# Kernel optimization log

Measured on AMD Instinct MI355X. Metric: run time of the kernel, lower is better.

The kernel has to match this reference:

```python
import jax, jax.numpy as jnp
import numpy as np

IFZ = 256      # in_features
SFZ = 1280     # sequence_features
AHZ = 8        # attention heads
AFZ = 64       # attention feature dim per head
NRES = 20      # canonical_num_residues
SCALE = float(np.sqrt(AFZ))
RESID = float(np.sqrt(2.0))
EPS = 1e-6


def _ln(x, s, b, eps=1e-5):
    m = jnp.mean(x, axis=-1, keepdims=True)
    v = jnp.var(x, axis=-1, keepdims=True)
    return (x - m) / jnp.sqrt(v + eps) * s + b


def setup_inputs() -> dict:
    key = jax.random.key(0)
    ks = jax.random.split(key, 20)
    N, B, S = 4096, 4, 512
    HD = AHZ * AFZ
    w = lambda k, shp: (jax.random.normal(k, shp, jnp.float32) * 0.02)
    d = {}
    d["x"] = jax.random.normal(ks[0], (N, IFZ), jnp.float32)
    d["packed_sequence_emb"] = jax.random.normal(ks[1], (B, S, SFZ), jnp.float32)
    d["packed_sequence_mask"] = jnp.ones((B, S), jnp.float32)
    d["prot_mask"] = jnp.arange(N, dtype=jnp.int32)
    d["batch"] = jax.random.randint(ks[2], (N,), 0, B, jnp.int32)
    # projections (bias=False)
    d["Wq"] = w(ks[3], (HD, IFZ))
    d["Wk"] = w(ks[4], (HD, SFZ))
    d["Wv"] = w(ks[5], (HD, SFZ))
    # ag: LayerNorm(HD) -> Linear(HD, IFZ, bias=False) (dropout = identity at eval)
    d["ag_ln_s"] = jnp.ones((HD,), jnp.float32)
    d["ag_ln_b"] = jnp.zeros((HD,), jnp.float32)
    d["Wag"] = w(ks[6], (IFZ, HD))
    d["res_ln_s"] = jnp.ones((3, IFZ), jnp.float32)
    d["res_ln_b"] = jnp.zeros((3, IFZ), jnp.float32)
    d["res_w1"] = w(ks[7], (3, IFZ, IFZ))
    d["res_b1"] = jnp.zeros((3, IFZ), jnp.float32)
    d["res_w2"] = w(ks[8], (3, IFZ, IFZ))
    d["res_b2"] = jnp.zeros((3, IFZ), jnp.float32)
    d["head_w"] = w(ks[9], (NRES, IFZ))
    d["head_b"] = jnp.zeros((NRES,), jnp.float32)
    # output LayerNorm en
    d["en_s"] = jnp.ones((IFZ,), jnp.float32)
    d["en_b"] = jnp.zeros((IFZ,), jnp.float32)
    return d


def _forward(x, emb, mask, prot_mask, batch, Wq, Wk, Wv, ag_ln_s, ag_ln_b, Wag,
             res_ln_s, res_ln_b, res_w1, res_b1, res_w2, res_b2,
             head_w, head_b, en_s, en_b):
    N = x.shape[0]
    B, S = emb.shape[:2]
    b_idx = batch[prot_mask]                      # [M]
    xp = x[prot_mask]                             # [M, IFZ]
    M = xp.shape[0]
    q = (xp @ Wq.T).reshape(M, AHZ, AFZ)          # [M,H,D]
    k = (emb @ Wk.T).reshape(B, S, AHZ, AFZ)      # [B,S,H,D]
    v = (emb @ Wv.T).reshape(B, S, AHZ, AFZ)
    # score vs every protein, then pick own protein (avoids materializing [M,S,H,D] gather)
    scores_all = jnp.einsum('mhd,bshd->mbsh', q, k) / SCALE          # [M,B,S,H]
    sel = b_idx[:, None, None, None]
    scores = jnp.take_along_axis(scores_all, sel, axis=1)[:, 0]       # [M,S,H]
    mb = mask[b_idx][:, :, None]                                      # [M,S,1]
    # padded_sequence_softmax: softmax over S, zero pads, renormalize
    sm = jax.nn.softmax(scores, axis=1) * mb
    w = sm / (jnp.sum(sm, axis=1, keepdims=True) + EPS)               # [M,S,H]
    feat_all = jnp.einsum('msh,bshd->mbhd', w, v)                     # [M,B,H,D]
    feat = jnp.take_along_axis(feat_all, sel, axis=1)[:, 0]
    feat = feat.reshape(M, AHZ * AFZ)
    ag = _ln(feat, ag_ln_s, ag_ln_b) @ Wag.T                          # [M, IFZ]
    # seq_aa_head on the scattered new features (identical to ag for unique prot_mask)
    h = ag
    for i in range(3):
        y = _ln(h, res_ln_s[i], res_ln_b[i])
        y = jax.nn.relu(y @ res_w1[i].T + res_b1[i])
        y = y @ res_w2[i].T + res_b2[i]
        h = (h + y) / RESID
    logits = h @ head_w.T + head_b                                     # [M, NRES]
    new_features = jnp.zeros_like(x).at[prot_mask].set(ag)
    seq_aa_logits = jnp.zeros((N, NRES), x.dtype).at[prot_mask].set(logits)
    unpacked_scores = jnp.zeros((N, S, AHZ), x.dtype).at[prot_mask].set(scores)
    out_x = _ln(x + new_features / RESID, en_s, en_b)
    return out_x, seq_aa_logits, unpacked_scores


def reference(x, packed_sequence_emb, packed_sequence_mask, prot_mask, batch,
              Wq, Wk, Wv, ag_ln_s, ag_ln_b, Wag,
              res_ln_s, res_ln_b, res_w1, res_b1, res_w2, res_b2,
              head_w, head_b, en_s, en_b):
    return _forward(x, packed_sequence_emb, packed_sequence_mask, prot_mask, batch,
                    Wq, Wk, Wv, ag_ln_s, ag_ln_b, Wag,
                    res_ln_s, res_ln_b, res_w1, res_b1, res_w2, res_b2,
                    head_w, head_b, en_s, en_b)
```

## Files before the change

### kernel.cpp

```cpp
#include <hip/hip_runtime.h>
#include <math.h>


typedef short bf8 __attribute__((ext_vector_type(8)));
typedef short bf4 __attribute__((ext_vector_type(4)));
typedef float f32x4 __attribute__((ext_vector_type(4)));
typedef unsigned short u16;

constexpr int LDT = 40;
enum { EPI_NONE = 0, EPI_BIAS_RELU = 1, EPI_BIAS = 2, EPI_RESID = 3 };
#define RSQRT2 0.70710678118654752f

__device__ __forceinline__ u16 f2bf(float f) {
  unsigned int u = __builtin_bit_cast(unsigned int, f);
  unsigned int r = u + 0x7fffu + ((u >> 16) & 1u);
  return (u16)(r >> 16);
}
__device__ __forceinline__ float bf2f(u16 v) {
  return __builtin_bit_cast(float, (unsigned int)v << 16);
}
__device__ __forceinline__ f32x4 mfma16(bf8 a, bf8 b, f32x4 c) {
  return __builtin_amdgcn_mfma_f32_16x16x32_bf16(a, b, c, 0, 0, 0);
}

struct CvtDesc { const float* src; u16* dst; int n; };
struct CvtArgs { CvtDesc d[8]; };

__global__ __launch_bounds__(256) void cvt_k(CvtArgs a) {
  CvtDesc d = a.d[blockIdx.z];
  int i = (blockIdx.x * 256 + threadIdx.x) * 8;
  if (i >= d.n) return;
  f32x4 v0 = *(const f32x4*)(d.src + i);
  f32x4 v1 = *(const f32x4*)(d.src + i + 4);
  bf8 o;
  o[0] = (short)f2bf(v0[0]); o[1] = (short)f2bf(v0[1]);
  o[2] = (short)f2bf(v0[2]); o[3] = (short)f2bf(v0[3]);
  o[4] = (short)f2bf(v1[0]); o[5] = (short)f2bf(v1[1]);
  o[6] = (short)f2bf(v1[2]); o[7] = (short)f2bf(v1[3]);
  *(bf8*)(d.dst + i) = o;
}

template <int EPI, bool BFOUT, int MT>
__global__ __launch_bounds__(256) void mgemm2(
    const u16* __restrict__ A, const u16* __restrict__ B,
    void* __restrict__ Cv, int M, int N, int K, int lda, int ldb, int ldc,
    const float* __restrict__ bias, const float* __restrict__ Hin,
    const int* __restrict__ gatherA, const int* __restrict__ scatterC) {
  constexpr int NF = MT / 32;
  __shared__ __align__(16) u16 As[MT * LDT];
  __shared__ __align__(16) u16 Bs[64 * LDT];
  const int tid = threadIdx.x;
  const int m0 = blockIdx.y * MT, n0 = blockIdx.x * 64;
  const int wave = tid >> 6, lane = tid & 63;
  const int wm = (wave & 1) * (MT / 2), wn = (wave >> 1) * 32;
  const int lrow = lane & 15, quad = lane >> 4;
  const int srow = tid >> 2, skq = tid & 3;

  int gr0 = m0 + srow;
  int ar0 = (gr0 < M) ? (gatherA ? gatherA[gr0] : gr0) : -1;
  const u16* Ap0 = (ar0 >= 0) ? A + (size_t)ar0 * lda + skq * 8 : nullptr;
  const u16* Ap1 = nullptr;
  if constexpr (MT == 128) {
    int gr1 = m0 + srow + 64;
    int ar1 = (gr1 < M) ? (gatherA ? gatherA[gr1] : gr1) : -1;
    Ap1 = (ar1 >= 0) ? A + (size_t)ar1 * lda + skq * 8 : nullptr;
  }
  const u16* Bp = (n0 + srow < N) ? B + (size_t)(n0 + srow) * ldb + skq * 8 : nullptr;
  u16* AsW0 = &As[srow * LDT + skq * 8];
  u16* AsW1 = (MT == 128) ? &As[(srow + 64) * LDT + skq * 8] : nullptr;
  u16* BsW = &Bs[srow * LDT + skq * 8];

  f32x4 acc[NF][2];
#pragma unroll
  for (int i = 0; i < NF; ++i)
#pragma unroll
    for (int j = 0; j < 2; ++j) acc[i][j] = (f32x4){0.f, 0.f, 0.f, 0.f};
  const bf8 z8 = {0, 0, 0, 0, 0, 0, 0, 0};

  for (int k0 = 0; k0 < K; k0 += 32) {
    bf8 a0 = Ap0 ? *(const bf8*)(Ap0 + k0) : z8;
    bf8 bv = Bp ? *(const bf8*)(Bp + k0) : z8;
    *(bf8*)AsW0 = a0;
    if constexpr (MT == 128) {
      bf8 a1 = Ap1 ? *(const bf8*)(Ap1 + k0) : z8;
      *(bf8*)AsW1 = a1;
    }
    *(bf8*)BsW = bv;
    __syncthreads();
    bf8 af[NF], bfr[2];
#pragma unroll
    for (int i = 0; i < NF; ++i)
      af[i] = *(const bf8*)&As[(wm + i * 16 + lrow) * LDT + quad * 8];
#pragma unroll
    for (int j = 0; j < 2; ++j)
      bfr[j] = *(const bf8*)&Bs[(wn + j * 16 + lrow) * LDT + quad * 8];
#pragma unroll
    for (int i = 0; i < NF; ++i)
#pragma unroll
      for (int j = 0; j < 2; ++j) acc[i][j] = mfma16(af[i], bfr[j], acc[i][j]);
    __syncthreads();
  }

  float* Cf = (float*)Cv;
  u16* Cb = (u16*)Cv;
#pragma unroll
  for (int i = 0; i < NF; ++i) {
#pragma unroll
    for (int r = 0; r < 4; ++r) {
      int row = m0 + wm + i * 16 + quad * 4 + r;
      if (row >= M) continue;
      if (gatherA && gatherA[row] < 0) continue;
      int orow = scatterC ? scatterC[row] : row;
#pragma unroll
      for (int j = 0; j < 2; ++j) {
        int col = n0 + wn + j * 16 + lrow;
        if (col >= N) continue;
        float v = acc[i][j][r];
        if (EPI == EPI_BIAS_RELU) v = fmaxf(v + bias[col], 0.f);
        else if (EPI == EPI_BIAS) v += bias[col];
        else if (EPI == EPI_RESID) v = (Hin[(size_t)row * ldc + col] + v + bias[col]) * RSQRT2;
        if (BFOUT) Cb[(size_t)orow * ldc + col] = f2bf(v);
        else Cf[(size_t)orow * ldc + col] = v;
      }
    }
  }
}

__global__ __launch_bounds__(256) void vtrans(const u16* __restrict__ KV,
                                              u16* __restrict__ VT) {
  __shared__ u16 t[32][33];
  int b = blockIdx.z;
  int s0 = blockIdx.x * 32, d0 = blockIdx.y * 32;
  int tx = threadIdx.x & 31, ty = threadIdx.x >> 5;
#pragma unroll
  for (int i = 0; i < 32; i += 8)
    t[ty + i][tx] = KV[(size_t)(b * 512 + s0 + ty + i) * 1024 + 512 + d0 + tx];
  __syncthreads();
#pragma unroll
  for (int i = 0; i < 32; i += 8)
    VT[(size_t)(b * 512 + d0 + ty + i) * 512 + s0 + tx] = t[tx][ty + i];
}

constexpr int WST = 520;
constexpr int QST = 72;

__global__ __launch_bounds__(256) void attn_fused(
    const u16* __restrict__ Q, const u16* __restrict__ KV,
    const u16* __restrict__ VT, const int* __restrict__ list,
    const float* __restrict__ mask, u16* __restrict__ packed,
    u16* __restrict__ feat, int N) {
  const int NMT = gridDim.x;
  const int lin = blockIdx.y * NMT + blockIdx.x;
  const int xcd = lin & 7, rest = lin >> 3;
  const int mt = rest % NMT;
  const int y = ((rest / NMT) << 3) | xcd;
  const int b = y >> 3, h = y & 7;
  const int* lst = list + (size_t)b * N + mt * 32;
  if (lst[0] < 0) return;

  __shared__ __align__(16) u16 Ws[32 * WST];
  __shared__ __align__(16) u16 KVs[2][64 * QST];
  __shared__ int mS[32];

  const int tid = threadIdx.x;
  const int wave = tid >> 6, lane = tid & 63;
  const int wm = (wave & 1) * 16, wns = (wave >> 1) * 32;
  const int lrow = lane & 15, quad = lane >> 4;
  const bf8 z8 = {0, 0, 0, 0, 0, 0, 0, 0};

  const int c0 = tid * 2, c1 = tid * 2 + 1;
  const int sr0 = c0 >> 3, kq0 = c0 & 7;
  const int sr1 = c1 >> 3, kq1 = c1 & 7;
  const int o0 = sr0 * QST + kq0 * 8, o1 = sr1 * QST + kq1 * 8;

  const u16* KVb = KV + (size_t)(b * 512) * 1024 + h * 64;
  const u16* VTb = VT + (size_t)(b * 512 + h * 64) * 512;

  if (tid < 32) mS[tid] = lst[tid];
  {
    int sta = mt & 7;
    *(bf8*)&KVs[0][o0] = *(const bf8*)(KVb + (size_t)(sta * 64 + sr0) * 1024 + kq0 * 8);
    *(bf8*)&KVs[0][o1] = *(const bf8*)(KVb + (size_t)(sta * 64 + sr1) * 1024 + kq1 * 8);
  }
  __syncthreads();

  const int qrow = mS[wm + lrow];
  const u16* Qr = Q + (size_t)qrow * 512 + h * 64 + quad * 8;
  const bf8 qa0 = (qrow >= 0) ? *(const bf8*)Qr : z8;
  const bf8 qa1 = (qrow >= 0) ? *(const bf8*)(Qr + 32) : z8;

  int cur = 0;
  bf8 r0, r1;
  for (int st = 0; st < 8; ++st) {
    const int sta = (st + mt) & 7;
    if (st < 7) {
      int nx = (st + 1 + mt) & 7;
      r0 = *(const bf8*)(KVb + (size_t)(nx * 64 + sr0) * 1024 + kq0 * 8);
      r1 = *(const bf8*)(KVb + (size_t)(nx * 64 + sr1) * 1024 + kq1 * 8);
    }
    f32x4 acc0 = {0.f, 0.f, 0.f, 0.f}, acc1 = acc0;
    {
      bf8 b00 = *(const bf8*)&KVs[cur][(wns + lrow) * QST + quad * 8];
      bf8 b10 = *(const bf8*)&KVs[cur][(wns + 16 + lrow) * QST + quad * 8];
      bf8 b01 = *(const bf8*)&KVs[cur][(wns + lrow) * QST + 32 + quad * 8];
      bf8 b11 = *(const bf8*)&KVs[cur][(wns + 16 + lrow) * QST + 32 + quad * 8];
      __builtin_amdgcn_s_setprio(1);
      acc0 = mfma16(qa0, b00, acc0);
      acc1 = mfma16(qa0, b10, acc1);
      acc0 = mfma16(qa1, b01, acc0);
      acc1 = mfma16(qa1, b11, acc1);
      __builtin_amdgcn_s_setprio(0);
    }
#pragma unroll
    for (int r = 0; r < 4; ++r) {
      int lr = wm + quad * 4 + r;
      Ws[lr * WST + sta * 64 + wns + lrow] = f2bf(acc0[r] * 0.125f);
      Ws[lr * WST + sta * 64 + wns + 16 + lrow] = f2bf(acc1[r] * 0.125f);
    }
    if (st < 7) {
      *(bf8*)&KVs[cur ^ 1][o0] = r0;
      *(bf8*)&KVs[cur ^ 1][o1] = r1;
    }
    __syncthreads();
    cur ^= 1;
  }

  bf8 v0p = *(const bf8*)(VTb + (size_t)sr0 * 512 + ((mt & 7) << 6) + kq0 * 8);
  bf8 v1p = *(const bf8*)(VTb + (size_t)sr1 * 512 + ((mt & 7) << 6) + kq1 * 8);

  {
    const int row = tid >> 3, part = tid & 7;
    u16* wrow = &Ws[row * WST + part * 64];
    const int mm = mS[row];
    const float* mkp = mask + (size_t)b * 512 + part * 64;
    bf8 w[8];
    float mx = -1e30f;
#pragma unroll
    for (int v = 0; v < 8; ++v) {
      w[v] = *(const bf8*)(wrow + v * 8);
#pragma unroll
      for (int j = 0; j < 8; ++j) mx = fmaxf(mx, bf2f((u16)w[v][j]));
    }
    if (mm >= 0) {
      u16* prow = packed + ((size_t)h * N + mm) * 512 + part * 64;
#pragma unroll
      for (int v = 0; v < 8; ++v) *(bf8*)(prow + v * 8) = w[v];
    }
#pragma unroll
    for (int d = 1; d < 8; d <<= 1) mx = fmaxf(mx, __shfl_xor(mx, d));
    float ev[64];
    float se = 0.f, ms = 0.f;
#pragma unroll
    for (int v = 0; v < 8; ++v) {
      f32x4 m0 = *(const f32x4*)(mkp + v * 8);
      f32x4 m1 = *(const f32x4*)(mkp + v * 8 + 4);
#pragma unroll
      for (int j = 0; j < 8; ++j) {
        float e = __expf(bf2f((u16)w[v][j]) - mx);
        ev[v * 8 + j] = e;
        se += e;
        ms += e * (j < 4 ? m0[j] : m1[j - 4]);
      }
    }
#pragma unroll
    for (int d = 1; d < 8; d <<= 1) {
      se += __shfl_xor(se, d);
      ms += __shfl_xor(ms, d);
    }
    float iv = 1.0f / (ms + 1e-6f * se);
#pragma unroll
    for (int v = 0; v < 8; ++v) {
      f32x4 m0 = *(const f32x4*)(mkp + v * 8);
      f32x4 m1 = *(const f32x4*)(mkp + v * 8 + 4);
      bf8 o;
#pragma unroll
      for (int j = 0; j < 8; ++j)
        o[j] = (short)f2bf(ev[v * 8 + j] * (j < 4 ? m0[j] : m1[j - 4]) * iv);
      *(bf8*)(wrow + v * 8) = o;
    }
  }
  __syncthreads();
  *(bf8*)&KVs[0][o0] = v0p;
  *(bf8*)&KVs[0][o1] = v1p;
  __syncthreads();

  f32x4 acc0 = {0.f, 0.f, 0.f, 0.f}, acc1 = acc0;
  cur = 0;
  for (int ss = 0; ss < 8; ++ss) {
    const int s0 = ((ss + mt) & 7) << 6;
    if (ss < 7) {
      int nx = ((ss + 1 + mt) & 7) << 6;
      v0p = *(const bf8*)(VTb + (size_t)sr0 * 512 + nx + kq0 * 8);
      v1p = *(const bf8*)(VTb + (size_t)sr1 * 512 + nx + kq1 * 8);
    }
#pragma unroll
    for (int k0 = 0; k0 < 64; k0 += 32) {
      bf8 a = *(const bf8*)&Ws[(wm + lrow) * WST + s0 + k0 + quad * 8];
      bf8 b0 = *(const bf8*)&KVs[cur][(wns + lrow) * QST + k0 + quad * 8];
      bf8 b1 = *(const bf8*)&KVs[cur][(wns + 16 + lrow) * QST + k0 + quad * 8];
      __builtin_amdgcn_s_setprio(1);
      acc0 = mfma16(a, b0, acc0);
      acc1 = mfma16(a, b1, acc1);
      __builtin_amdgcn_s_setprio(0);
    }
    if (ss < 7) {
      *(bf8*)&KVs[cur ^ 1][o0] = v0p;
      *(bf8*)&KVs[cur ^ 1][o1] = v1p;
      __syncthreads();
    }
    cur ^= 1;
  }
#pragma unroll
  for (int r = 0; r < 4; ++r) {
    int lr = wm + quad * 4 + r;
    int mm = mS[lr];
    if (mm < 0) continue;
    u16* frow = feat + (size_t)mm * 512 + h * 64;
    frow[wns + lrow] = f2bf(acc0[r]);
    frow[wns + 16 + lrow] = f2bf(acc1[r]);
  }
}

__global__ __launch_bounds__(256) void unpack_k(const u16* __restrict__ packed,
                                                const int* __restrict__ pm,
                                                float* __restrict__ out_sc,
                                                int N) {
  __shared__ u16 Ls[8 * 520];
  int m = blockIdx.x, tid = threadIdx.x;
  int h = tid >> 5, c = (tid & 31) * 16;
  const u16* row = packed + ((size_t)h * N + m) * 512 + c;
  *(bf8*)&Ls[h * 520 + c] = *(const bf8*)row;
  *(bf8*)&Ls[h * 520 + c + 8] = *(const bf8*)(row + 8);
  __syncthreads();
  float* orow = out_sc + (size_t)pm[m] * 4096;
#pragma unroll
  for (int i = 0; i < 16; ++i) {
    int e = tid + i * 256;
    orow[e] = bf2f(Ls[(e & 7) * 520 + (e >> 3)]);
  }
}

constexpr int HST = 268;
constexpr int AST = 520;
constexpr int YST = 280;

__global__ __launch_bounds__(1024) void mlp_fused(
    const u16* __restrict__ feat, const float* __restrict__ ag_s,
    const float* __restrict__ ag_b, const u16* __restrict__ Wag,
    const float* __restrict__ x, const float* __restrict__ ens,
    const float* __restrict__ enb, const float* __restrict__ rls,
    const float* __restrict__ rlb, const u16* __restrict__ rw1,
    const float* __restrict__ rb1, const u16* __restrict__ rw2,
    const float* __restrict__ rb2, const float* __restrict__ hw,
    const float* __restrict__ hb, const int* __restrict__ pm,
    float* __restrict__ out_lg, float* __restrict__ out_x) {
  __shared__ __align__(16) float Hs[16 * HST];
  __shared__ __align__(16) u16 As[16 * AST];
  __shared__ __align__(16) u16 Ys[16 * YST];
  const int tid = threadIdx.x;
  const int m0 = blockIdx.x * 16;
  const int wave = tid >> 6, lane = tid & 63;
  const int lrow = lane & 15, quad = lane >> 4;
  const int wn = wave * 16;
  const int row = wave;
  const int wq8 = quad * 8;
  const int nrow = pm[m0 + row];

  const u16* WagW = Wag + (size_t)(wn + lrow) * 512 + wq8;
  const u16* W1W = rw1 + (size_t)(wn + lrow) * 256 + wq8;
  const u16* W2W = rw2 + (size_t)(wn + lrow) * 256 + wq8;

  bf8 wp[8];
#pragma unroll
  for (int i = 0; i < 8; ++i) wp[i] = *(const bf8*)(WagW + i * 32);

  {
    const u16* frow = feat + (size_t)(m0 + row) * 512 + lane * 8;
    bf8 f0 = *(const bf8*)frow;
    float s = 0.f, sq = 0.f;
#pragma unroll
    for (int j = 0; j < 8; ++j) {
      float a = bf2f((u16)f0[j]);
      s += a;
      sq += a * a;
    }
#pragma unroll
    for (int d = 1; d < 64; d <<= 1) { s += __shfl_xor(s, d); sq += __shfl_xor(sq, d); }
    float mean = s * (1.0f / 512.0f);
    float var = sq * (1.0f / 512.0f) - mean * mean;
    float is = 1.0f / sqrtf(var + 1e-5f);
    int c = lane * 8;
    bf8 o0;
#pragma unroll
    for (int j = 0; j < 8; ++j)
      o0[j] = (short)f2bf((bf2f((u16)f0[j]) - mean) * is * ag_s[c + j] + ag_b[c + j]);
    *(bf8*)&As[row * AST + c] = o0;
  }
  __syncthreads();

  {
    f32x4 acc = {0.f, 0.f, 0.f, 0.f};
#pragma unroll
    for (int i = 0; i < 8; ++i) {
      bf8 a = *(const bf8*)&As[lrow * AST + i * 32 + wq8];
      acc = mfma16(a, wp[i], acc);
      wp[i] = *(const bf8*)(WagW + 256 + i * 32);
    }
#pragma unroll
    for (int i = 0; i < 8; ++i) {
      bf8 a = *(const bf8*)&As[lrow * AST + 256 + i * 32 + wq8];
      acc = mfma16(a, wp[i], acc);
      wp[i] = *(const bf8*)(W1W + i * 32);
    }
#pragma unroll
    for (int r = 0; r < 4; ++r) {
      int rr = quad * 4 + r;
      Hs[rr * HST + wn + lrow] = acc[r];
    }
  }
  __syncthreads();

  {
    int c = lane * 4;
    f32x4 xv = *(const f32x4*)&x[(size_t)nrow * 256 + c];
    f32x4 hv = *(const f32x4*)&Hs[row * HST + c];
    f32x4 v;
#pragma unroll
    for (int e = 0; e < 4; ++e) v[e] = xv[e] + hv[e] * RSQRT2;
    float s = v[0] + v[1] + v[2] + v[3];
    float sq = v[0] * v[0] + v[1] * v[1] + v[2] * v[2] + v[3] * v[3];
#pragma unroll
    for (int d = 1; d < 64; d <<= 1) { s += __shfl_xor(s, d); sq += __shfl_xor(sq, d); }
    float mean = s * (1.0f / 256.0f);
    float var = sq * (1.0f / 256.0f) - mean * mean;
    float is = 1.0f / sqrtf(var + 1e-5f);
    f32x4 o;
#pragma unroll
    for (int e = 0; e < 4; ++e)
      o[e] = (v[e] - mean) * is * ens[c + e] + enb[c + e];
    *(f32x4*)&out_x[(size_t)nrow * 256 + c] = o;
  }

  for (int layer = 0; layer < 3; ++layer) {
    {
      int c = lane * 4;
      f32x4 h0 = *(const f32x4*)&Hs[row * HST + c];
      float s = h0[0] + h0[1] + h0[2] + h0[3];
      float sq = h0[0] * h0[0] + h0[1] * h0[1] + h0[2] * h0[2] + h0[3] * h0[3];
#pragma unroll
      for (int d = 1; d < 64; d <<= 1) { s += __shfl_xor(s, d); sq += __shfl_xor(sq, d); }
      float mean = s * (1.0f / 256.0f);
      float var = sq * (1.0f / 256.0f) - mean * mean;
      float is = 1.0f / sqrtf(var + 1e-5f);
      const float* g = rls + layer * 256;
      const float* bb = rlb + layer * 256;
      bf4 o;
#pragma unroll
      for (int e = 0; e < 4; ++e)
        o[e] = (short)f2bf((h0[e] - mean) * is * g[c + e] + bb[c + e]);
      *(bf4*)&As[row * AST + c] = o;
    }
    __syncthreads();

    {
      f32x4 acc = {0.f, 0.f, 0.f, 0.f};
#pragma unroll
      for (int i = 0; i < 8; ++i) {
        bf8 a = *(const bf8*)&As[lrow * AST + i * 32 + wq8];
        acc = mfma16(a, wp[i], acc);
        wp[i] = *(const bf8*)(W2W + (size_t)layer * 65536 + i * 32);
      }
      float bi = rb1[layer * 256 + wn + lrow];
#pragma unroll
      for (int r = 0; r < 4; ++r) {
        int rr = quad * 4 + r;
        Ys[rr * YST + wn + lrow] = f2bf(fmaxf(acc[r] + bi, 0.f));
      }
    }
    __syncthreads();

    {
      f32x4 acc = {0.f, 0.f, 0.f, 0.f};
#pragma unroll
      for (int i = 0; i < 8; ++i) {
        bf8 a = *(const bf8*)&Ys[lrow * YST + i * 32 + wq8];
        acc = mfma16(a, wp[i], acc);
        if (layer < 2)
          wp[i] = *(const bf8*)(W1W + (size_t)(layer + 1) * 65536 + i * 32);
      }
      float bi = rb2[layer * 256 + wn + lrow];
#pragma unroll
      for (int r = 0; r < 4; ++r) {
        int rr = quad * 4 + r;
        float* h0 = &Hs[rr * HST + wn + lrow];
        *h0 = (*h0 + acc[r] + bi) * RSQRT2;
      }
    }
    __syncthreads();
  }

  if (lane < 20) {
    const float* hrow = &Hs[row * HST];
    const float* wrow = hw + (size_t)lane * 256;
    float l0 = 0.f, l1 = 0.f, l2 = 0.f, l3 = 0.f;
    for (int k = 0; k < 256; k += 16) {
      f32x4 h0 = *(const f32x4*)&hrow[k];
      f32x4 h1 = *(const f32x4*)&hrow[k + 4];
      f32x4 h2 = *(const f32x4*)&hrow[k + 8];
      f32x4 h3 = *(const f32x4*)&hrow[k + 12];
      f32x4 w0 = *(const f32x4*)&wrow[k];
      f32x4 w1 = *(const f32x4*)&wrow[k + 4];
      f32x4 w2 = *(const f32x4*)&wrow[k + 8];
      f32x4 w3 = *(const f32x4*)&wrow[k + 12];
#pragma unroll
      for (int e = 0; e < 4; ++e) {
        l0 += h0[e] * w0[e];
        l1 += h1[e] * w1[e];
        l2 += h2[e] * w2[e];
        l3 += h3[e] * w3[e];
      }
    }
    out_lg[(size_t)nrow * 20 + lane] = l0 + l1 + l2 + l3 + hb[lane];
  }
}

__global__ __launch_bounds__(256) void outx_k(
    const float* __restrict__ x, const int* __restrict__ inv,
    const float* __restrict__ g, const float* __restrict__ bb,
    float* __restrict__ out) {
  __shared__ float red[256];
  int n = blockIdx.x, tid = threadIdx.x;
  if (inv[n] >= 0) return;
  float v = x[(size_t)n * 256 + tid];
  red[tid] = v;
  __syncthreads();
  for (int off = 128; off; off >>= 1) {
    if (tid < off) red[tid] += red[tid + off];
    __syncthreads();
  }
  float mean = red[0] * (1.0f / 256.0f);
  __syncthreads();
  red[tid] = v * v;
  __syncthreads();
  for (int off = 128; off; off >>= 1) {
    if (tid < off) red[tid] += red[tid + off];
    __syncthreads();
  }
  float var = red[0] * (1.0f / 256.0f) - mean * mean;
  float is = 1.0f / sqrtf(var + 1e-5f);
  out[(size_t)n * 256 + tid] = (v - mean) * is * g[tid] + bb[tid];
}

__global__ void init_idx_k(int* __restrict__ list, int* __restrict__ inv,
                           int* __restrict__ cnt, int N, int B) {
  int i = blockIdx.x * 256 + threadIdx.x;
  if (i < B * N) list[i] = -1;
  if (i < N) inv[i] = -1;
  if (i < B) cnt[i] = 0;
}

__global__ void compact_k(const int* __restrict__ pm,
                          const int* __restrict__ batch, int* __restrict__ list,
                          int* __restrict__ inv, int* __restrict__ cnt, int N) {
  int m = blockIdx.x * 256 + threadIdx.x;
  if (m >= N) return;
  int p = pm[m];
  int b = batch[p];
  int slot = atomicAdd(&cnt[b], 1);
  list[(size_t)b * N + slot] = m;
  inv[p] = m;
}

extern "C" void kernel_launch(void* const* d_in, const int* in_sizes, int n_in,
                              void* d_out, int out_size, void* d_ws,
                              size_t ws_size, hipStream_t stream) {
  const float* x = (const float*)d_in[0];
  const float* emb = (const float*)d_in[1];
  const float* mask = (const float*)d_in[2];
  const int* pm = (const int*)d_in[3];
  const int* batch = (const int*)d_in[4];
  const float* Wq = (const float*)d_in[5];
  const float* Wk = (const float*)d_in[6];
  const float* Wv = (const float*)d_in[7];
  const float* ag_s = (const float*)d_in[8];
  const float* ag_b = (const float*)d_in[9];
  const float* Wag = (const float*)d_in[10];
  const float* rls = (const float*)d_in[11];
  const float* rlb = (const float*)d_in[12];
  const float* rw1 = (const float*)d_in[13];
  const float* rb1 = (const float*)d_in[14];
  const float* rw2 = (const float*)d_in[15];
  const float* rb2 = (const float*)d_in[16];
  const float* hw = (const float*)d_in[17];
  const float* hb = (const float*)d_in[18];
  const float* ens = (const float*)d_in[19];
  const float* enb = (const float*)d_in[20];

  const int N = in_sizes[0] / 256;
  const int B = in_sizes[2] / 512;

  char* wsb = (char*)d_ws;
  u16* embbf = (u16*)(wsb + 0);
  u16* xbf   = (u16*)(wsb + 5242880);
  u16* Wkvbf = (u16*)(wsb + 7340032);
  u16* Wqbf  = (u16*)(wsb + 9961472);
  u16* packed = (u16*)(wsb + 0);
  u16* KVbf   = (u16*)(wsb + 33554432);
  u16* Qbf    = (u16*)(wsb + 37748736);
  u16* VT     = (u16*)(wsb + 41943040);
  u16* featE  = (u16*)(wsb + 44040192);
  u16* Wagbf = (u16*)(wsb + 48234496);
  u16* rw1bf = (u16*)(wsb + 48496640);
  u16* rw2bf = (u16*)(wsb + 48889856);
  int* list  = (int*)(wsb + 49545216);
  int* inv   = (int*)(wsb + 49610752);
  int* cnt   = (int*)(wsb + 49627136);

  float* out_x = (float*)d_out;
  float* out_lg = out_x + (size_t)N * 256;
  float* out_sc = out_lg + (size_t)N * 20;

  CvtArgs ca;
  ca.d[0] = {emb, embbf, 2 * 512 * 1280 * 2};
  ca.d[1] = {x, xbf, 4096 * 256};
  ca.d[2] = {Wk, Wkvbf, 512 * 1280};
  ca.d[3] = {Wv, Wkvbf + 512 * 1280, 512 * 1280};
  ca.d[4] = {Wq, Wqbf, 512 * 256};
  ca.d[5] = {Wag, Wagbf, 256 * 512};
  ca.d[6] = {rw1, rw1bf, 3 * 256 * 256};
  ca.d[7] = {rw2, rw2bf, 3 * 256 * 256};
  cvt_k<<<dim3(1281, 1, 8), 256, 0, stream>>>(ca);
  init_idx_k<<<(B * N + 255) / 256, 256, 0, stream>>>(list, inv, cnt, N, B);
  compact_k<<<(N + 255) / 256, 256, 0, stream>>>(pm, batch, list, inv, cnt, N);

  mgemm2<EPI_NONE, true, 64><<<dim3(16, B * 8), 256, 0, stream>>>(
      embbf, Wkvbf, KVbf, B * 512, 1024, 1280, 1280, 1280, 1024,
      nullptr, nullptr, nullptr, nullptr);
  mgemm2<EPI_NONE, true, 64><<<dim3(8, N / 64), 256, 0, stream>>>(
      xbf, Wqbf, Qbf, N, 512, 256, 256, 256, 512,
      nullptr, nullptr, pm, nullptr);
  vtrans<<<dim3(16, 16, B), 256, 0, stream>>>(KVbf, VT);

  attn_fused<<<dim3(N / 32, B * 8), 256, 0, stream>>>(
      Qbf, KVbf, VT, list, mask, packed, featE, N);
  unpack_k<<<N, 256, 0, stream>>>(packed, pm, out_sc, N);

  mlp_fused<<<dim3(N / 16), 1024, 0, stream>>>(
      featE, ag_s, ag_b, Wagbf, x, ens, enb, rls, rlb, rw1bf, rb1,
      rw2bf, rb2, hw, hb, pm, out_lg, out_x);

  outx_k<<<N, 256, 0, stream>>>(x, inv, ens, enb, out_x);
}
```

Before: 293.6 us.

## Halve mlp_fused rows per block, give each wave two 16-column output tiles

The fused MLP kernel now processes 8 rows per block with 8 waves (512 threads) instead of 16 rows with 16 waves, doubling the grid to 512 blocks. Each wave computes two 16-wide output column tiles and reuses one A fragment across two MFMAs. Rows 8-15 of each MFMA tile are duplicates and their results are discarded. The aim is more blocks for better CU coverage and overlap, at the cost of wasting half the MFMA work, doubling per-wave weight register traffic, and reloading the weights for twice as many blocks.

```diff
diff --git a/kernel.cpp b/kernel.cpp
--- a/kernel.cpp
+++ b/kernel.cpp
@@ -344,7 +344,7 @@
 constexpr int AST = 520;
 constexpr int YST = 280;
 
-__global__ __launch_bounds__(1024) void mlp_fused(
+__global__ __launch_bounds__(512, 4) void mlp_fused(
     const u16* __restrict__ feat, const float* __restrict__ ag_s,
     const float* __restrict__ ag_b, const u16* __restrict__ Wag,
     const float* __restrict__ x, const float* __restrict__ ens,
@@ -354,25 +354,32 @@
     const float* __restrict__ rb2, const float* __restrict__ hw,
     const float* __restrict__ hb, const int* __restrict__ pm,
     float* __restrict__ out_lg, float* __restrict__ out_x) {
-  __shared__ __align__(16) float Hs[16 * HST];
-  __shared__ __align__(16) u16 As[16 * AST];
-  __shared__ __align__(16) u16 Ys[16 * YST];
+  __shared__ __align__(16) float Hs[8 * HST];
+  __shared__ __align__(16) u16 As[8 * AST];
+  __shared__ __align__(16) u16 Ys[8 * YST];
   const int tid = threadIdx.x;
-  const int m0 = blockIdx.x * 16;
+  const int m0 = blockIdx.x * 8;
   const int wave = tid >> 6, lane = tid & 63;
   const int lrow = lane & 15, quad = lane >> 4;
-  const int wn = wave * 16;
+  const int ar = lrow & 7;
+  const int wn = wave * 32;
   const int row = wave;
   const int wq8 = quad * 8;
   const int nrow = pm[m0 + row];
 
-  const u16* WagW = Wag + (size_t)(wn + lrow) * 512 + wq8;
-  const u16* W1W = rw1 + (size_t)(wn + lrow) * 256 + wq8;
-  const u16* W2W = rw2 + (size_t)(wn + lrow) * 256 + wq8;
-
-  bf8 wp[8];
-#pragma unroll
-  for (int i = 0; i < 8; ++i) wp[i] = *(const bf8*)(WagW + i * 32);
+  const u16* Wag0 = Wag + (size_t)(wn + lrow) * 512 + wq8;
+  const u16* Wag1 = Wag + (size_t)(wn + 16 + lrow) * 512 + wq8;
+  const u16* W1a = rw1 + (size_t)(wn + lrow) * 256 + wq8;
+  const u16* W1b = rw1 + (size_t)(wn + 16 + lrow) * 256 + wq8;
+  const u16* W2a = rw2 + (size_t)(wn + lrow) * 256 + wq8;
+  const u16* W2b = rw2 + (size_t)(wn + 16 + lrow) * 256 + wq8;
+
+  bf8 wp0[8], wp1[8];
+#pragma unroll
+  for (int i = 0; i < 8; ++i) {
+    wp0[i] = *(const bf8*)(Wag0 + i * 32);
+    wp1[i] = *(const bf8*)(Wag1 + i * 32);
+  }
 
   {
     const u16* frow = feat + (size_t)(m0 + row) * 512 + lane * 8;
@@ -399,23 +406,30 @@
   __syncthreads();
 
   {
-    f32x4 acc = {0.f, 0.f, 0.f, 0.f};
+    f32x4 acc0 = {0.f, 0.f, 0.f, 0.f}, acc1 = acc0;
 #pragma unroll
     for (int i = 0; i < 8; ++i) {
-      bf8 a = *(const bf8*)&As[lrow * AST + i * 32 + wq8];
-      acc = mfma16(a, wp[i], acc);
-      wp[i] = *(const bf8*)(WagW + 256 + i * 32);
+      bf8 a = *(const bf8*)&As[ar * AST + i * 32 + wq8];
+      acc0 = mfma16(a, wp0[i], acc0);
+      acc1 = mfma16(a, wp1[i], acc1);
+      wp0[i] = *(const bf8*)(Wag0 + 256 + i * 32);
+      wp1[i] = *(const bf8*)(Wag1 + 256 + i * 32);
     }
 #pragma unroll
     for (int i = 0; i < 8; ++i) {
-      bf8 a = *(const bf8*)&As[lrow * AST + 256 + i * 32 + wq8];
-      acc = mfma16(a, wp[i], acc);
-      wp[i] = *(const bf8*)(W1W + i * 32);
+      bf8 a = *(const bf8*)&As[ar * AST + 256 + i * 32 + wq8];
+      acc0 = mfma16(a, wp0[i], acc0);
+      acc1 = mfma16(a, wp1[i], acc1);
+      wp0[i] = *(const bf8*)(W1a + i * 32);
+      wp1[i] = *(const bf8*)(W1b + i * 32);
     }
 #pragma unroll
     for (int r = 0; r < 4; ++r) {
       int rr = quad * 4 + r;
-      Hs[rr * HST + wn + lrow] = acc[r];
+      if (rr < 8) {
+        Hs[rr * HST + wn + lrow] = acc0[r];
+        Hs[rr * HST + wn + 16 + lrow] = acc1[r];
+      }
     }
   }
   __syncthreads();
@@ -463,37 +477,51 @@
     __syncthreads();
 
     {
-      f32x4 acc = {0.f, 0.f, 0.f, 0.f};
+      f32x4 acc0 = {0.f, 0.f, 0.f, 0.f}, acc1 = acc0;
 #pragma unroll
       for (int i = 0; i < 8; ++i) {
-        bf8 a = *(const bf8*)&As[lrow * AST + i * 32 + wq8];
-        acc = mfma16(a, wp[i], acc);
-        wp[i] = *(const bf8*)(W2W + (size_t)layer * 65536 + i * 32);
-      }
-      float bi = rb1[layer * 256 + wn + lrow];
+        bf8 a = *(const bf8*)&As[ar * AST + i * 32 + wq8];
+        acc0 = mfma16(a, wp0[i], acc0);
+        acc1 = mfma16(a, wp1[i], acc1);
+        wp0[i] = *(const bf8*)(W2a + (size_t)layer * 65536 + i * 32);
+        wp1[i] = *(const bf8*)(W2b + (size_t)layer * 65536 + i * 32);
+      }
+      float bi0 = rb1[layer * 256 + wn + lrow];
+      float bi1 = rb1[layer * 256 + wn + 16 + lrow];
 #pragma unroll
       for (int r = 0; r < 4; ++r) {
         int rr = quad * 4 + r;
-        Ys[rr * YST + wn + lrow] = f2bf(fmaxf(acc[r] + bi, 0.f));
+        if (rr < 8) {
+          Ys[rr * YST + wn + lrow] = f2bf(fmaxf(acc0[r] + bi0, 0.f));
+          Ys[rr * YST + wn + 16 + lrow] = f2bf(fmaxf(acc1[r] + bi1, 0.f));
+        }
       }
     }
     __syncthreads();
 
     {
-      f32x4 acc = {0.f, 0.f, 0.f, 0.f};
+      f32x4 acc0 = {0.f, 0.f, 0.f, 0.f}, acc1 = acc0;
 #pragma unroll
       for (int i = 0; i < 8; ++i) {
-        bf8 a = *(const bf8*)&Ys[lrow * YST + i * 32 + wq8];
-        acc = mfma16(a, wp[i], acc);
-        if (layer < 2)
-          wp[i] = *(const bf8*)(W1W + (size_t)(layer + 1) * 65536 + i * 32);
-      }
-      float bi = rb2[layer * 256 + wn + lrow];
+        bf8 a = *(const bf8*)&Ys[ar * YST + i * 32 + wq8];
+        acc0 = mfma16(a, wp0[i], acc0);
+        acc1 = mfma16(a, wp1[i], acc1);
+        if (layer < 2) {
+          wp0[i] = *(const bf8*)(W1a + (size_t)(layer + 1) * 65536 + i * 32);
+          wp1[i] = *(const bf8*)(W1b + (size_t)(layer + 1) * 65536 + i * 32);
+        }
+      }
+      float bi0 = rb2[layer * 256 + wn + lrow];
+      float bi1 = rb2[layer * 256 + wn + 16 + lrow];
 #pragma unroll
       for (int r = 0; r < 4; ++r) {
         int rr = quad * 4 + r;
-        float* h0 = &Hs[rr * HST + wn + lrow];
-        *h0 = (*h0 + acc[r] + bi) * RSQRT2;
+        if (rr < 8) {
+          float* h0 = &Hs[rr * HST + wn + lrow];
+          float* h1 = &Hs[rr * HST + wn + 16 + lrow];
+          *h0 = (*h0 + acc0[r] + bi0) * RSQRT2;
+          *h1 = (*h1 + acc1[r] + bi1) * RSQRT2;
+        }
       }
     }
     __syncthreads();
@@ -645,7 +673,7 @@
       Qbf, KVbf, VT, list, mask, packed, featE, N);
   unpack_k<<<N, 256, 0, stream>>>(packed, pm, out_sc, N);
 
-  mlp_fused<<<dim3(N / 16), 1024, 0, stream>>>(
+  mlp_fused<<<dim3(N / 8), 512, 0, stream>>>(
       featE, ag_s, ag_b, Wagbf, x, ens, enb, rls, rlb, rw1bf, rb1,
       rw2bf, rb2, hw, hb, pm, out_lg, out_x);
 
```

Result: slower. 329.2 us (+12.1%).
